# Kernel optimization log

Measured on AMD Instinct MI355X. Metric: run time of the kernel, lower is better.

Reference implementation:

```python
import jax, jax.numpy as jnp
import numpy as np

EPS = 1e-5   # BatchNorm3d eps
SLOPE = 0.01 # LeakyReLU default negative_slope

def conv3(x, w, pad):
    return jax.lax.conv_general_dilated(
        x, w, (1, 1, 1), [(pad, pad)] * 3,
        dimension_numbers=('NCDHW', 'OIDHW', 'NCDHW'))

def bn(x):
    # BatchNorm3d in training mode with affine init (weight=1, bias=0):
    # normalize by per-channel batch statistics (biased variance).
    m = x.mean(axis=(0, 2, 3, 4), keepdims=True)
    v = x.var(axis=(0, 2, 3, 4), keepdims=True)
    return (x - m) / jnp.sqrt(v + EPS)

def lrelu(x):
    return jnp.where(x >= 0, x, SLOPE * x)

def block(x, w1, w2):
    # ConvBlock: conv3x3x3 -> BN -> LeakyReLU, twice
    x = lrelu(bn(conv3(x, w1, 1)))
    return lrelu(bn(conv3(x, w2, 1)))

def maxpool2(x):
    # MaxPool3dMPS(kernel=2, stride=2, pad=0) == standard 2x2x2 maxpool
    B, C, D, H, W = x.shape
    return x.reshape(B, C, D // 2, 2, H // 2, 2, W // 2, 2).max(axis=(3, 5, 7))

def upconv_fft(x, w):
    # ConvTranspose3dMPS: nearest-neighbor upsample by stride=2 via repeat,
    # then per-(out,in)-channel CIRCULAR convolution implemented with FFTs
    # (weight zero-padded to the upsampled spatial shape). Vectorized here
    # over all channel pairs with a frequency-domain einsum; rfft is used
    # since all signals are real (identical math, half the memory).
    s = 2
    B, C, D, H, W = x.shape
    up = jnp.broadcast_to(x[:, :, :, None, :, None, :, None],
                          (B, C, D, s, H, s, W, s)).reshape(B, C, D * s, H * s, W * s)
    sp = up.shape[2:]
    X = jnp.fft.rfftn(up, axes=(2, 3, 4))                 # [B, Cin, D', H', Wf]
    Wf = jnp.fft.rfftn(w, s=sp, axes=(2, 3, 4))           # [Cout, Cin, D', H', Wf]
    Y = jnp.einsum('bidhw,oidhw->bodhw', X, Wf)
    return jnp.fft.irfftn(Y, s=sp, axes=(2, 3, 4))

def unet_fwd(x, wf1, wf2, wd1a, wd1b, wd2a, wd2b, wd3a, wd3b,
             wt1, wu1a, wu1b, wt2, wu2a, wu2b, wt3, wu3a, wu3b,
             w_final, b_final):
    x1 = block(x, wf1, wf2)                       # [B,16,64,64,64]
    x2 = block(maxpool2(x1), wd1a, wd1b)          # [B,32,32,32,32]
    x3 = block(maxpool2(x2), wd2a, wd2b)          # [B,64,16,16,16]
    x4 = block(maxpool2(x3), wd3a, wd3b)          # [B,128,8,8,8]

    def up(a, skip, wt, wa, wb):
        u = lrelu(bn(upconv_fft(a, wt)))
        return block(jnp.concatenate([skip, u], axis=1), wa, wb)

    a = up(x4, x3, wt1, wu1a, wu1b)               # [B,64,16,16,16]
    a = up(a, x2, wt2, wu2a, wu2b)                # [B,32,32,32,32]
    a = up(a, x1, wt3, wu3a, wu3b)                # [B,16,64,64,64]
    return conv3(a, w_final, 0) + b_final.reshape(1, -1, 1, 1, 1)

def setup_inputs() -> dict:
    key = jax.random.key(0)
    ks = jax.random.split(key, 32)
    def W(k, shape):
        fan = int(np.prod(shape[1:]))
        return jax.random.normal(k, shape, jnp.float32) * np.float32((2.0 / fan) ** 0.5)
    inp = {}
    inp['x'] = jax.random.normal(ks[0], (1, 1, 64, 64, 64), jnp.float32)
    shapes = {
        'wf1': (16, 1, 3, 3, 3),  'wf2': (16, 16, 3, 3, 3),
        'wd1a': (32, 16, 3, 3, 3), 'wd1b': (32, 32, 3, 3, 3),
        'wd2a': (64, 32, 3, 3, 3), 'wd2b': (64, 64, 3, 3, 3),
        'wd3a': (128, 64, 3, 3, 3), 'wd3b': (128, 128, 3, 3, 3),
        'wt1': (64, 128, 2, 2, 2), 'wu1a': (64, 128, 3, 3, 3), 'wu1b': (64, 64, 3, 3, 3),
        'wt2': (32, 64, 2, 2, 2),  'wu2a': (32, 64, 3, 3, 3),  'wu2b': (32, 32, 3, 3, 3),
        'wt3': (16, 32, 2, 2, 2),  'wu3a': (16, 32, 3, 3, 3),  'wu3b': (16, 16, 3, 3, 3),
        'w_final': (1, 16, 1, 1, 1),
    }
    for i, (name, sh) in enumerate(shapes.items()):
        inp[name] = W(ks[i + 1], sh)
    inp['b_final'] = jnp.zeros((1,), jnp.float32)
    return inp

def reference(x, wf1, wf2, wd1a, wd1b, wd2a, wd2b, wd3a, wd3b,
              wt1, wu1a, wu1b, wt2, wu2a, wu2b, wt3, wu3a, wu3b,
              w_final, b_final):
    return unet_fwd(x, wf1, wf2, wd1a, wd1b, wd2a, wd2b, wd3a, wd3b,
                    wt1, wu1a, wu1b, wt2, wu2a, wu2b, wt3, wu3a, wu3b,
                    w_final, b_final)
```

## Files before the change

### kernel.cpp

```cpp
#include <hip/hip_runtime.h>

#define EPS   1e-5f
#define SLOPE 0.01f

template <int CIN, int BT>
__global__ __launch_bounds__(BT) void conv3_big(const float* __restrict__ in,
                                                const float* __restrict__ wt,
                                                float* __restrict__ out,
                                                float* __restrict__ bstat,
                                                int D, int H, int W) {
    const int V   = D * H * W;
    const int NB  = gridDim.y;
    const int co0 = blockIdx.x * 8;
    __shared__ float wlds[27 * CIN * 8];
    __shared__ float sred[(BT / 64) * 16];
    for (int i = threadIdx.x; i < 27 * CIN * 8; i += BT) {
        const int co  = i & 7;
        const int r   = i >> 3;
        const int tap = r % 3;
        const int r2  = r / 3;
        const int pl  = r2 % 9;
        const int ci  = r2 / 9;
        wlds[i] = wt[((size_t)(co0 + co) * CIN + ci) * 27 + pl * 3 + tap];
    }
    __syncthreads();

    const int v0 = (blockIdx.y * BT + threadIdx.x) * 4;
    const int w0 = v0 % W;
    const int h0 = (v0 / W) % H;
    const int d0 = v0 / (W * H);
    const bool mL = (w0 != 0);
    const bool mR = (w0 + 4 != W);
    const int  wl = w0 - (mL ? 1 : 0);
    const int  wr = w0 + (mR ? 4 : 3);

    float acc[32];
#pragma unroll
    for (int i = 0; i < 32; ++i) acc[i] = 0.f;

#pragma unroll 1
    for (int ci = 0; ci < CIN; ++ci) {
        const float* pc = in + (size_t)ci * V;
#pragma unroll
        for (int kd = 0; kd < 3; ++kd) {
#pragma unroll
            for (int kh = 0; kh < 3; ++kh) {
                const int zd = d0 + kd - 1, zh = h0 + kh - 1;
                const bool okp = ((unsigned)zd < (unsigned)D) & ((unsigned)zh < (unsigned)H);
                const int row = okp ? (zd * H + zh) * W : 0;
                const float* p = pc + row;
                float4 m = *(const float4*)(p + w0);
                float lv = p[wl];
                float rv = p[wr];
                if (!okp) { m.x = 0.f; m.y = 0.f; m.z = 0.f; m.w = 0.f; }
                if (!(okp && mL)) lv = 0.f;
                if (!(okp && mR)) rv = 0.f;
                const float* wb = &wlds[((ci * 9 + kd * 3 + kh) * 3) * 8];
                const float4 t0a = *(const float4*)(wb);
                const float4 t0b = *(const float4*)(wb + 4);
                const float4 t1a = *(const float4*)(wb + 8);
                const float4 t1b = *(const float4*)(wb + 12);
                const float4 t2a = *(const float4*)(wb + 16);
                const float4 t2b = *(const float4*)(wb + 20);
#define FMA4C(A0, A1, A2, AP)                                                       \
                {                                                                   \
                    float* a = (AP);                                                \
                    a[0] = fmaf(lv,  (A0), fmaf(m.x, (A1), fmaf(m.y, (A2), a[0]))); \
                    a[1] = fmaf(m.x, (A0), fmaf(m.y, (A1), fmaf(m.z, (A2), a[1]))); \
                    a[2] = fmaf(m.y, (A0), fmaf(m.z, (A1), fmaf(m.w, (A2), a[2]))); \
                    a[3] = fmaf(m.z, (A0), fmaf(m.w, (A1), fmaf(rv,  (A2), a[3]))); \
                }
                FMA4C(t0a.x, t1a.x, t2a.x, acc + 0);
                FMA4C(t0a.y, t1a.y, t2a.y, acc + 4);
                FMA4C(t0a.z, t1a.z, t2a.z, acc + 8);
                FMA4C(t0a.w, t1a.w, t2a.w, acc + 12);
                FMA4C(t0b.x, t1b.x, t2b.x, acc + 16);
                FMA4C(t0b.y, t1b.y, t2b.y, acc + 20);
                FMA4C(t0b.z, t1b.z, t2b.z, acc + 24);
                FMA4C(t0b.w, t1b.w, t2b.w, acc + 28);
#undef FMA4C
            }
        }
    }
#pragma unroll
    for (int co = 0; co < 8; ++co)
        *(float4*)&out[(size_t)(co0 + co) * V + v0] = *(const float4*)&acc[co * 4];

    float s1[8], s2[8];
#pragma unroll
    for (int co = 0; co < 8; ++co) {
        const float* a = &acc[co * 4];
        s1[co] = a[0] + a[1] + a[2] + a[3];
        s2[co] = fmaf(a[0], a[0], fmaf(a[1], a[1], fmaf(a[2], a[2], a[3] * a[3])));
    }
#pragma unroll
    for (int off = 32; off > 0; off >>= 1)
#pragma unroll
        for (int co = 0; co < 8; ++co) {
            s1[co] += __shfl_down(s1[co], off, 64);
            s2[co] += __shfl_down(s2[co], off, 64);
        }
    const int lane = threadIdx.x & 63;
    const int wv   = threadIdx.x >> 6;
    if (lane == 0)
#pragma unroll
        for (int co = 0; co < 8; ++co) {
            sred[(wv * 8 + co) * 2]     = s1[co];
            sred[(wv * 8 + co) * 2 + 1] = s2[co];
        }
    __syncthreads();
    if ((int)threadIdx.x < 8) {
        float S1 = 0.f, S2 = 0.f;
#pragma unroll
        for (int w = 0; w < BT / 64; ++w) {
            S1 += sred[(w * 8 + threadIdx.x) * 2];
            S2 += sred[(w * 8 + threadIdx.x) * 2 + 1];
        }
        bstat[((size_t)(co0 + threadIdx.x) * NB + blockIdx.y) * 2]     = S1;
        bstat[((size_t)(co0 + threadIdx.x) * NB + blockIdx.y) * 2 + 1] = S2;
    }
}

template <int CIN>
__global__ __launch_bounds__(256) void upconv_big(const float* __restrict__ in,
                                                  const float* __restrict__ wt,
                                                  float* __restrict__ out,
                                                  float* __restrict__ bstat,
                                                  int Di, int Hi, int Wi) {
    const int Do = 2 * Di, Ho = 2 * Hi, Wo = 2 * Wi;
    const int Vo = Do * Ho * Wo;
    const int Vi = Di * Hi * Wi;
    const int NB = gridDim.y;
    const int co0 = blockIdx.x * 8;
    __shared__ float wlds[8 * CIN * 8];
    __shared__ float sred[4 * 16];
    for (int i = threadIdx.x; i < 8 * CIN * 8; i += 256) {
        const int co  = i & 7;
        const int t2  = i >> 3;
        const int ci  = t2 % CIN;
        const int tap = t2 / CIN;
        wlds[i] = wt[((size_t)(co0 + co) * CIN + ci) * 8 + tap];
    }
    __syncthreads();

    const int vbase = blockIdx.y * 1024 + threadIdx.x;
    int od[4], oh[4], ow[4];
#pragma unroll
    for (int j = 0; j < 4; ++j) {
        const int v = vbase + j * 256;
        ow[j] = v % Wo;
        oh[j] = (v / Wo) % Ho;
        od[j] = v / (Wo * Ho);
    }
    float acc[32];
#pragma unroll
    for (int i = 0; i < 32; ++i) acc[i] = 0.f;

#pragma unroll 1
    for (int kd = 0; kd < 2; ++kd)
#pragma unroll 1
    for (int kh = 0; kh < 2; ++kh)
#pragma unroll
    for (int kw = 0; kw < 2; ++kw) {
        const int tap = (kd * 2 + kh) * 2 + kw;
        int sp[4];
#pragma unroll
        for (int j = 0; j < 4; ++j) {
            const int id = ((od[j] - kd + Do) & (Do - 1)) >> 1;
            const int ih = ((oh[j] - kh + Ho) & (Ho - 1)) >> 1;
            const int iw = ((ow[j] - kw + Wo) & (Wo - 1)) >> 1;
            sp[j] = (id * Hi + ih) * Wi + iw;
        }
        const float* wrow = &wlds[tap * CIN * 8];
#pragma unroll 2
        for (int ci = 0; ci < CIN; ++ci) {
            float xv[4];
#pragma unroll
            for (int j = 0; j < 4; ++j)
                xv[j] = in[(size_t)ci * Vi + sp[j]];
            const float4 wa = *(const float4*)(wrow + ci * 8);
            const float4 wb = *(const float4*)(wrow + ci * 8 + 4);
#define UF(WC, CO)                                                              \
            {                                                                   \
                _Pragma("unroll")                                               \
                for (int j = 0; j < 4; ++j)                                     \
                    acc[(CO) * 4 + j] = fmaf(xv[j], (WC), acc[(CO) * 4 + j]);   \
            }
            UF(wa.x, 0) UF(wa.y, 1) UF(wa.z, 2) UF(wa.w, 3)
            UF(wb.x, 4) UF(wb.y, 5) UF(wb.z, 6) UF(wb.w, 7)
#undef UF
        }
    }
#pragma unroll
    for (int co = 0; co < 8; ++co)
#pragma unroll
        for (int j = 0; j < 4; ++j)
            out[(size_t)(co0 + co) * Vo + vbase + j * 256] = acc[co * 4 + j];

    float s1[8], s2[8];
#pragma unroll
    for (int co = 0; co < 8; ++co) {
        const float* a = &acc[co * 4];
        s1[co] = a[0] + a[1] + a[2] + a[3];
        s2[co] = fmaf(a[0], a[0], fmaf(a[1], a[1], fmaf(a[2], a[2], a[3] * a[3])));
    }
#pragma unroll
    for (int off = 32; off > 0; off >>= 1)
#pragma unroll
        for (int co = 0; co < 8; ++co) {
            s1[co] += __shfl_down(s1[co], off, 64);
            s2[co] += __shfl_down(s2[co], off, 64);
        }
    const int lane = threadIdx.x & 63;
    const int wv   = threadIdx.x >> 6;
    if (lane == 0)
#pragma unroll
        for (int co = 0; co < 8; ++co) {
            sred[(wv * 8 + co) * 2]     = s1[co];
            sred[(wv * 8 + co) * 2 + 1] = s2[co];
        }
    __syncthreads();
    if ((int)threadIdx.x < 8) {
        float S1 = 0.f, S2 = 0.f;
#pragma unroll
        for (int w = 0; w < 4; ++w) {
            S1 += sred[(w * 8 + threadIdx.x) * 2];
            S2 += sred[(w * 8 + threadIdx.x) * 2 + 1];
        }
        bstat[((size_t)(co0 + threadIdx.x) * NB + blockIdx.y) * 2]     = S1;
        bstat[((size_t)(co0 + threadIdx.x) * NB + blockIdx.y) * 2 + 1] = S2;
    }
}

__global__ __launch_bounds__(256) void bn_apply_f(const float* __restrict__ prt,
                                                  float* __restrict__ dst,
                                                  const float* __restrict__ bstat,
                                                  int NB, int V4, float invV) {
    const int c = blockIdx.x;
    float s1 = 0.f, s2 = 0.f;
    for (int i = threadIdx.x; i < NB; i += 256) {
        s1 += bstat[((size_t)c * NB + i) * 2];
        s2 += bstat[((size_t)c * NB + i) * 2 + 1];
    }
#pragma unroll
    for (int off = 32; off > 0; off >>= 1) {
        s1 += __shfl_down(s1, off, 64);
        s2 += __shfl_down(s2, off, 64);
    }
    __shared__ float sh[8];
    __shared__ float mv[2];
    const int lane = threadIdx.x & 63;
    const int wv   = threadIdx.x >> 6;
    if (lane == 0) { sh[wv] = s1; sh[4 + wv] = s2; }
    __syncthreads();
    if (threadIdx.x == 0) {
        const float S1 = sh[0] + sh[1] + sh[2] + sh[3];
        const float S2 = sh[4] + sh[5] + sh[6] + sh[7];
        const float mean = S1 * invV;
        const float var  = S2 * invV - mean * mean;
        mv[0] = mean;
        mv[1] = rsqrtf(var + EPS);
    }
    __syncthreads();
    const float mean = mv[0];
    const float rstd = mv[1];
    const int pos = blockIdx.y * 256 + threadIdx.x;
    float4 t = ((const float4*)prt)[(size_t)c * V4 + pos];
    float u;
    u = (t.x - mean) * rstd; t.x = u >= 0.f ? u : SLOPE * u;
    u = (t.y - mean) * rstd; t.y = u >= 0.f ? u : SLOPE * u;
    u = (t.z - mean) * rstd; t.z = u >= 0.f ? u : SLOPE * u;
    u = (t.w - mean) * rstd; t.w = u >= 0.f ? u : SLOPE * u;
    ((float4*)dst)[(size_t)c * V4 + pos] = t;
}

template <int CIN, int CC, int BT>
__global__ __launch_bounds__(BT) void conv3_qA(const float* __restrict__ in,
                                               const float* __restrict__ wt,
                                               float* __restrict__ part,
                                               int D, int H, int W) {
    const int V    = D * H * W;
    const int Cout = gridDim.x * 8;
    const int z    = blockIdx.z;
    const int cib  = z * CC;
    __shared__ float wlds[27 * CC * 8];
    const int co0 = blockIdx.x * 8;
    for (int i = threadIdx.x; i < 27 * CC * 8; i += BT) {
        const int co  = i & 7;
        const int t2  = i >> 3;
        const int tap = t2 % 3;
        const int t3  = t2 / 3;
        const int ci  = t3 % CC;
        const int pl  = t3 / CC;
        wlds[i] = wt[((size_t)(co0 + co) * CIN + cib + ci) * 27 + pl * 3 + tap];
    }
    __syncthreads();

    const float* inz = in + (size_t)cib * V;
    const int v0 = (blockIdx.y * BT + threadIdx.x) * 4;
    const int w0 = v0 % W;
    const int h0 = (v0 / W) % H;
    const int d0 = v0 / (W * H);

    const bool mL = (w0 != 0);
    const bool mR = (w0 + 4 != W);
    const int  wl = w0 - (mL ? 1 : 0);
    const int  wr = w0 + (mR ? 4 : 3);

    float acc[32];
#pragma unroll
    for (int i = 0; i < 32; ++i) acc[i] = 0.f;

#pragma unroll 1
    for (int kd = 0; kd < 3; ++kd) {
#pragma unroll 1
        for (int kh = 0; kh < 3; ++kh) {
            const int zd = d0 + kd - 1, zh = h0 + kh - 1;
            const bool okp = ((unsigned)zd < (unsigned)D) & ((unsigned)zh < (unsigned)H);
            const int row = okp ? (zd * H + zh) * W : 0;
            const float* wpl = &wlds[(kd * 3 + kh) * CC * 24];
#pragma unroll 2
            for (int ci = 0; ci < CC; ++ci) {
                const float* p = inz + (size_t)ci * V + row;
                float4 m = *(const float4*)(p + w0);
                float lv = p[wl];
                float rv = p[wr];
                if (!okp) { m.x = 0.f; m.y = 0.f; m.z = 0.f; m.w = 0.f; }
                if (!(okp && mL)) lv = 0.f;
                if (!(okp && mR)) rv = 0.f;
                const float* wb = wpl + ci * 24;
                const float4 t0a = *(const float4*)(wb);
                const float4 t0b = *(const float4*)(wb + 4);
                const float4 t1a = *(const float4*)(wb + 8);
                const float4 t1b = *(const float4*)(wb + 12);
                const float4 t2a = *(const float4*)(wb + 16);
                const float4 t2b = *(const float4*)(wb + 20);
#define FMA4C(A0, A1, A2, AP)                                                       \
                {                                                                   \
                    float* a = (AP);                                                \
                    a[0] = fmaf(lv,  (A0), fmaf(m.x, (A1), fmaf(m.y, (A2), a[0]))); \
                    a[1] = fmaf(m.x, (A0), fmaf(m.y, (A1), fmaf(m.z, (A2), a[1]))); \
                    a[2] = fmaf(m.y, (A0), fmaf(m.z, (A1), fmaf(m.w, (A2), a[2]))); \
                    a[3] = fmaf(m.z, (A0), fmaf(m.w, (A1), fmaf(rv,  (A2), a[3]))); \
                }
                FMA4C(t0a.x, t1a.x, t2a.x, acc + 0);
                FMA4C(t0a.y, t1a.y, t2a.y, acc + 4);
                FMA4C(t0a.z, t1a.z, t2a.z, acc + 8);
                FMA4C(t0a.w, t1a.w, t2a.w, acc + 12);
                FMA4C(t0b.x, t1b.x, t2b.x, acc + 16);
                FMA4C(t0b.y, t1b.y, t2b.y, acc + 20);
                FMA4C(t0b.z, t1b.z, t2b.z, acc + 24);
                FMA4C(t0b.w, t1b.w, t2b.w, acc + 28);
#undef FMA4C
            }
        }
    }
#pragma unroll
    for (int co = 0; co < 8; ++co)
        *(float4*)&part[((size_t)z * Cout + co0 + co) * V + v0] = *(const float4*)&acc[co * 4];
}

template <int CIN, int CC, int VOXB>
__global__ __launch_bounds__(256) void upconv_v8(const float* __restrict__ in,
                                                 const float* __restrict__ wt,
                                                 float* __restrict__ part,
                                                 int Di, int Hi, int Wi) {
    const int Do = 2 * Di, Ho = 2 * Hi, Wo = 2 * Wi;
    const int Vo = Do * Ho * Wo;
    const int Vi = Di * Hi * Wi;
    const int Cout = gridDim.x * 8;
    const int z    = blockIdx.z;
    const int cib  = z * CC;
    __shared__ float wlds[8 * CC * 8];
    const int co0 = blockIdx.x * 8;
    for (int i = threadIdx.x; i < 8 * CC * 8; i += 256) {
        const int co  = i & 7;
        const int t2  = i >> 3;
        const int ci  = t2 % CC;
        const int tap = t2 / CC;
        wlds[i] = wt[((size_t)(co0 + co) * CIN + cib + ci) * 8 + tap];
    }
    __syncthreads();

    const float* inz = in + (size_t)cib * Vi;
    const int vbase = blockIdx.y * (256 * VOXB) + threadIdx.x;
    int od[VOXB], oh[VOXB], ow[VOXB];
#pragma unroll
    for (int j = 0; j < VOXB; ++j) {
        const int v = vbase + j * 256;
        ow[j] = v % Wo;
        oh[j] = (v / Wo) % Ho;
        od[j] = v / (Wo * Ho);
    }
    float acc[8 * VOXB];
#pragma unroll
    for (int i = 0; i < 8 * VOXB; ++i) acc[i] = 0.f;

#pragma unroll 1
    for (int kd = 0; kd < 2; ++kd)
#pragma unroll 1
    for (int kh = 0; kh < 2; ++kh)
#pragma unroll
    for (int kw = 0; kw < 2; ++kw) {
        const int tap = (kd * 2 + kh) * 2 + kw;
        int sp[VOXB];
#pragma unroll
        for (int j = 0; j < VOXB; ++j) {
            const int id = ((od[j] - kd + Do) & (Do - 1)) >> 1;
            const int ih = ((oh[j] - kh + Ho) & (Ho - 1)) >> 1;
            const int iw = ((ow[j] - kw + Wo) & (Wo - 1)) >> 1;
            sp[j] = (id * Hi + ih) * Wi + iw;
        }
        const float* wrow = &wlds[tap * CC * 8];
#pragma unroll 2
        for (int ci = 0; ci < CC; ++ci) {
            float xv[VOXB];
#pragma unroll
            for (int j = 0; j < VOXB; ++j)
                xv[j] = inz[(size_t)ci * Vi + sp[j]];
            const float4 wa = *(const float4*)(wrow + ci * 8);
            const float4 wb = *(const float4*)(wrow + ci * 8 + 4);
#define UF(WC, CO)                                                              \
            {                                                                   \
                _Pragma("unroll")                                               \
                for (int j = 0; j < VOXB; ++j)                                  \
                    acc[(CO) * VOXB + j] = fmaf(xv[j], (WC), acc[(CO) * VOXB + j]); \
            }
            UF(wa.x, 0) UF(wa.y, 1) UF(wa.z, 2) UF(wa.w, 3)
            UF(wb.x, 4) UF(wb.y, 5) UF(wb.z, 6) UF(wb.w, 7)
#undef UF
        }
    }
#pragma unroll
    for (int co = 0; co < 8; ++co)
#pragma unroll
        for (int j = 0; j < VOXB; ++j)
            part[((size_t)z * Cout + co0 + co) * Vo + vbase + j * 256] = acc[co * VOXB + j];
}

__global__ __launch_bounds__(256) void bn_stats_part_v2(const float* __restrict__ part,
                                                        float* __restrict__ pstat,
                                                        int C, int V, int S, int chunk) {
    const int c = blockIdx.x, seg = blockIdx.y;
    const size_t base = (size_t)c * V + (size_t)seg * chunk;
    float s1 = 0.f, s2 = 0.f;
    for (int i = threadIdx.x * 4; i < chunk; i += 1024) {
        float4 t = make_float4(0.f, 0.f, 0.f, 0.f);
        for (int s = 0; s < S; ++s) {
            const float4 v = *(const float4*)(part + (size_t)s * C * V + base + i);
            t.x += v.x; t.y += v.y; t.z += v.z; t.w += v.w;
        }
        s1 += t.x + t.y + t.z + t.w;
        s2 = fmaf(t.x, t.x, fmaf(t.y, t.y, fmaf(t.z, t.z, fmaf(t.w, t.w, s2))));
    }
#pragma unroll
    for (int off = 32; off > 0; off >>= 1) {
        s1 += __shfl_down(s1, off, 64);
        s2 += __shfl_down(s2, off, 64);
    }
    __shared__ float sh[8];
    const int wid  = threadIdx.x >> 6;
    const int lane = threadIdx.x & 63;
    if (lane == 0) { sh[wid] = s1; sh[4 + wid] = s2; }
    __syncthreads();
    if (threadIdx.x == 0) {
        pstat[(c * gridDim.y + seg) * 2]     = sh[0] + sh[1] + sh[2] + sh[3];
        pstat[(c * gridDim.y + seg) * 2 + 1] = sh[4] + sh[5] + sh[6] + sh[7];
    }
}

__global__ __launch_bounds__(64) void bn_stats_final(const float* __restrict__ pstat,
                                                     float* __restrict__ stats,
                                                     int S, int V) {
    const int c = blockIdx.x;
    float s1 = 0.f, s2 = 0.f;
    if ((int)threadIdx.x < S) {
        s1 = pstat[(c * S + threadIdx.x) * 2];
        s2 = pstat[(c * S + threadIdx.x) * 2 + 1];
    }
#pragma unroll
    for (int off = 32; off > 0; off >>= 1) {
        s1 += __shfl_down(s1, off, 64);
        s2 += __shfl_down(s2, off, 64);
    }
    if (threadIdx.x == 0) {
        const float inv  = 1.f / (float)V;
        const float mean = s1 * inv;
        const float var  = s2 * inv - mean * mean;
        stats[2 * c]     = mean;
        stats[2 * c + 1] = rsqrtf(var + EPS);
    }
}

__global__ __launch_bounds__(256) void bn_apply_v3(const float* __restrict__ part,
                                                   float* __restrict__ dst,
                                                   const float* __restrict__ stats,
                                                   int C, int V4, int S, int total4) {
    const int idx = blockIdx.x * blockDim.x + threadIdx.x;
    if (idx >= total4) return;
    const int c = idx / V4;
    const int v = idx - c * V4;
    const float4* p4 = (const float4*)part;
    float4 t = make_float4(0.f, 0.f, 0.f, 0.f);
    for (int s = 0; s < S; ++s) {
        const float4 x = p4[(size_t)(s * C + c) * V4 + v];
        t.x += x.x; t.y += x.y; t.z += x.z; t.w += x.w;
    }
    const float mean = stats[2 * c];
    const float rstd = stats[2 * c + 1];
    float u;
    u = (t.x - mean) * rstd; t.x = u >= 0.f ? u : SLOPE * u;
    u = (t.y - mean) * rstd; t.y = u >= 0.f ? u : SLOPE * u;
    u = (t.z - mean) * rstd; t.z = u >= 0.f ? u : SLOPE * u;
    u = (t.w - mean) * rstd; t.w = u >= 0.f ? u : SLOPE * u;
    ((float4*)dst)[idx] = t;
}

__global__ __launch_bounds__(256) void maxpool_kernel(const float* __restrict__ in,
                                                      float* __restrict__ out,
                                                      int D, int H, int W, int total) {
    const int Do = D >> 1, Ho = H >> 1, Wo = W >> 1;
    const int Vo = Do * Ho * Wo;
    const int idx = blockIdx.x * blockDim.x + threadIdx.x;
    if (idx >= total) return;
    const int c  = idx / Vo;
    const int v  = idx - c * Vo;
    const int ow = v % Wo;
    const int oh = (v / Wo) % Ho;
    const int od = v / (Wo * Ho);
    const size_t HW = (size_t)H * W;
    const float* p = in + (size_t)c * D * HW + (size_t)(2 * od) * HW + (size_t)(2 * oh) * W + 2 * ow;
    float m = p[0];
    m = fmaxf(m, p[1]);
    m = fmaxf(m, p[W]);
    m = fmaxf(m, p[W + 1]);
    m = fmaxf(m, p[HW]);
    m = fmaxf(m, p[HW + 1]);
    m = fmaxf(m, p[HW + W]);
    m = fmaxf(m, p[HW + W + 1]);
    out[idx] = m;
}

__global__ __launch_bounds__(256) void final_v2(const float* __restrict__ in,
                                                const float* __restrict__ w,
                                                const float* __restrict__ b,
                                                float* __restrict__ out, int C, int V4) {
    const int idx = blockIdx.x * blockDim.x + threadIdx.x;
    if (idx >= V4) return;
    const float bb = b[0];
    float4 acc = make_float4(bb, bb, bb, bb);
    for (int c = 0; c < C; ++c) {
        const float4 v = ((const float4*)in)[(size_t)c * V4 + idx];
        const float wc = w[c];
        acc.x = fmaf(v.x, wc, acc.x);
        acc.y = fmaf(v.y, wc, acc.y);
        acc.z = fmaf(v.z, wc, acc.z);
        acc.w = fmaf(v.w, wc, acc.w);
    }
    ((float4*)out)[idx] = acc;
}


extern "C" void kernel_launch(void* const* d_in, const int* in_sizes, int n_in,
                              void* d_out, int out_size, void* d_ws, size_t ws_size,
                              hipStream_t stream) {
    const float* x      = (const float*)d_in[0];
    const float* wf1    = (const float*)d_in[1];
    const float* wf2    = (const float*)d_in[2];
    const float* wd1a   = (const float*)d_in[3];
    const float* wd1b   = (const float*)d_in[4];
    const float* wd2a   = (const float*)d_in[5];
    const float* wd2b   = (const float*)d_in[6];
    const float* wd3a   = (const float*)d_in[7];
    const float* wd3b   = (const float*)d_in[8];
    const float* wt1    = (const float*)d_in[9];
    const float* wu1a   = (const float*)d_in[10];
    const float* wu1b   = (const float*)d_in[11];
    const float* wt2    = (const float*)d_in[12];
    const float* wu2a   = (const float*)d_in[13];
    const float* wu2b   = (const float*)d_in[14];
    const float* wt3    = (const float*)d_in[15];
    const float* wu3a   = (const float*)d_in[16];
    const float* wu3b   = (const float*)d_in[17];
    const float* w_fin  = (const float*)d_in[18];
    const float* b_fin  = (const float*)d_in[19];
    float* out = (float*)d_out;

    const int V0 = 64 * 64 * 64;
    const int V1 = 32 * 32 * 32;
    const int V2 = 16 * 16 * 16;
    const int V3 = 8 * 8 * 8;

    float* ws    = (float*)d_ws;
    float* cat3  = ws;
    float* cat2  = cat3 + (size_t)32 * V0;
    float* cat1  = cat2 + (size_t)64 * V1;
    float* x4    = cat1 + (size_t)128 * V2;
    float* tA    = x4   + (size_t)128 * V3;
    float* tB    = tA   + (size_t)16 * V0;
    float* part  = tB   + (size_t)16 * V0;
    float* stats = part + (size_t)16 * V0;
    float* pstat = stats + 256;
    float* bstat = pstat + 4096;

    auto blocks = [](int n) { return (n + 255) / 256; };

    auto bn_lrelu = [&](const float* p, float* dstp, int C, int V, int S) {
        const int NSEG = (V >= V0) ? 16 : (V == V1) ? 8 : (V == V2) ? 2 : 1;
        hipLaunchKernelGGL(bn_stats_part_v2, dim3(C, NSEG), dim3(256), 0, stream,
                           p, pstat, C, V, S, V / NSEG);
        hipLaunchKernelGGL(bn_stats_final, dim3(C), dim3(64), 0, stream, pstat, stats, NSEG, V);
        const int total4 = C * V / 4;
        hipLaunchKernelGGL(bn_apply_v3, dim3(blocks(total4)), dim3(256), 0, stream,
                           p, dstp, stats, C, V / 4, S, total4);
    };
    auto maxpool = [&](const float* in, float* o, int C, int D, int H, int W) {
        const int total = C * (D / 2) * (H / 2) * (W / 2);
        hipLaunchKernelGGL(maxpool_kernel, dim3(blocks(total)), dim3(256), 0, stream,
                           in, o, D, H, W, total);
    };

#define CONVBIG(CIN, in_, wt_, prt_, dst_, Cout)                                            \
    {                                                                                       \
        const int NBv = V0 / (4 * 128);                                                     \
        dim3 g((Cout) / 8, NBv);                                                            \
        hipLaunchKernelGGL((conv3_big<CIN, 128>), g, dim3(128), 0, stream,                  \
                           in_, wt_, prt_, bstat, 64, 64, 64);                              \
        hipLaunchKernelGGL(bn_apply_f, dim3(Cout, V0 / 4 / 256), dim3(256), 0, stream,      \
                           prt_, dst_, bstat, NBv, V0 / 4, 1.f / V0);                       \
    }
#define CONVQ(CIN, CC, BT, in_, wt_, prt_, dst_, Cout, D_, H_, W_)                          \
    {                                                                                       \
        const int V_ = (D_) * (H_) * (W_);                                                  \
        const int S  = (CIN) / (CC);                                                        \
        dim3 g((Cout) / 8, V_ / (4 * (BT)), S);                                             \
        hipLaunchKernelGGL((conv3_qA<CIN, CC, BT>), g, dim3(BT), 0, stream,                 \
                           in_, wt_, prt_, D_, H_, W_);                                     \
        bn_lrelu(prt_, dst_, Cout, V_, S);                                                  \
    }
#define UPCONV(CIN, CC, VOXB, in_, wt_, prt_, dst_, Cout, Di_, Hi_, Wi_)                    \
    {                                                                                       \
        const int Vo_ = 8 * (Di_) * (Hi_) * (Wi_);                                          \
        const int S  = (CIN) / (CC);                                                        \
        dim3 g((Cout) / 8, Vo_ / (256 * (VOXB)), S);                                        \
        hipLaunchKernelGGL((upconv_v8<CIN, CC, VOXB>), g, dim3(256), 0, stream,             \
                           in_, wt_, prt_, Di_, Hi_, Wi_);                                  \
        bn_lrelu(prt_, dst_, Cout, Vo_, S);                                                 \
    }

    CONVBIG(1,  x,  wf1, tA, tA,   16);
    CONVBIG(16, tA, wf2, tB, cat3, 16);
    maxpool(cat3, tA, 16, 64, 64, 64);
    CONVQ(16,  8,  64,  tA,  wd1a, part, tB,          32, 32, 32, 32);
    CONVQ(32,  8,  64,  tB,  wd1b, part, cat2,        32, 32, 32, 32);
    maxpool(cat2, tA, 32, 32, 32, 32);
    CONVQ(32,  8,  64,  tA,  wd2a, part, tB,          64, 16, 16, 16);
    CONVQ(64,  8,  64,  tB,  wd2b, part, cat1,        64, 16, 16, 16);
    maxpool(cat1, tA, 64, 16, 16, 16);
    CONVQ(64,  4,  64,  tA,  wd3a, part, tB,         128, 8, 8, 8);
    CONVQ(128, 8,  64,  tB,  wd3b, part, x4,         128, 8, 8, 8);

    UPCONV(128, 16, 1, x4, wt1, part, cat1 + (size_t)64 * V2, 64, 8, 8, 8);
    CONVQ(128, 8,  64, cat1, wu1a, part, tA,          64, 16, 16, 16);
    CONVQ(64,  8,  64, tA,   wu1b, part, tB,          64, 16, 16, 16);

    UPCONV(64, 16, 1, tB, wt2, part, cat2 + (size_t)32 * V1, 32, 16, 16, 16);
    CONVQ(64, 16, 64, cat2, wu2a, part, tA,           32, 32, 32, 32);
    CONVQ(32, 8,  64, tA,   wu2b, part, tB,           32, 32, 32, 32);

    {
        float* up3dst = cat3 + (size_t)16 * V0;
        const int NBv = V0 / 1024;
        dim3 g(2, NBv);
        hipLaunchKernelGGL((upconv_big<32>), g, dim3(256), 0, stream,
                           tB, wt3, up3dst, bstat, 32, 32, 32);
        hipLaunchKernelGGL(bn_apply_f, dim3(16, V0 / 4 / 256), dim3(256), 0, stream,
                           up3dst, up3dst, bstat, NBv, V0 / 4, 1.f / V0);
    }
    CONVBIG(32, cat3, wu3a, tB,   tA, 16);
    CONVBIG(16, tA,   wu3b, cat3, tB, 16);

    hipLaunchKernelGGL(final_v2, dim3(blocks(V0 / 4)), dim3(256), 0, stream,
                       tB, w_fin, b_fin, out, 16, V0 / 4);

#undef CONVBIG
#undef CONVQ
#undef UPCONV
}
```

Baseline: 1.098 ms.

## Stage conv input halo tiles in LDS and fold BN stat finalize into apply

The 64^3 3x3x3 conv kernel now cooperatively loads a 3x10x64 input halo tile per input channel into shared memory. All 9 row taps then read neighbours from LDS instead of issuing separate global loads, at the cost of two barriers per channel. Separately, the bn_stats_final launch is removed: each bn_apply thread re-reduces the per-segment partial sums and computes mean and rstd itself. This saves one launch per BN but adds redundant small loads in every thread.

```diff
diff --git a/kernel.cpp b/kernel.cpp
--- a/kernel.cpp
+++ b/kernel.cpp
@@ -3,18 +3,18 @@
 #define EPS   1e-5f
 #define SLOPE 0.01f
 
-template <int CIN, int BT>
-__global__ __launch_bounds__(BT) void conv3_big(const float* __restrict__ in,
-                                                const float* __restrict__ wt,
-                                                float* __restrict__ out,
-                                                float* __restrict__ bstat,
-                                                int D, int H, int W) {
-    const int V   = D * H * W;
+template <int CIN>
+__global__ __launch_bounds__(128) void conv3_big(const float* __restrict__ in,
+                                                 const float* __restrict__ wt,
+                                                 float* __restrict__ out,
+                                                 float* __restrict__ bstat) {
+    const int V   = 64 * 64 * 64;
     const int NB  = gridDim.y;
     const int co0 = blockIdx.x * 8;
     __shared__ float wlds[27 * CIN * 8];
-    __shared__ float sred[(BT / 64) * 16];
-    for (int i = threadIdx.x; i < 27 * CIN * 8; i += BT) {
+    __shared__ float tile[3][10][64];
+    __shared__ float sred[2 * 16];
+    for (int i = threadIdx.x; i < 27 * CIN * 8; i += 128) {
         const int co  = i & 7;
         const int r   = i >> 3;
         const int tap = r % 3;
@@ -23,16 +23,15 @@
         const int ci  = r2 / 9;
         wlds[i] = wt[((size_t)(co0 + co) * CIN + ci) * 27 + pl * 3 + tap];
     }
-    __syncthreads();
-
-    const int v0 = (blockIdx.y * BT + threadIdx.x) * 4;
-    const int w0 = v0 % W;
-    const int h0 = (v0 / W) % H;
-    const int d0 = v0 / (W * H);
+
+    const int vb    = blockIdx.y * 512;
+    const int d0    = vb >> 12;
+    const int hbase = (vb >> 6) & 63;
+    const int hh0   = threadIdx.x >> 4;
+    const int w0    = (threadIdx.x & 15) * 4;
+    const int v0    = vb + (hh0 * 64) + w0;
     const bool mL = (w0 != 0);
-    const bool mR = (w0 + 4 != W);
-    const int  wl = w0 - (mL ? 1 : 0);
-    const int  wr = w0 + (mR ? 4 : 3);
+    const bool mR = (w0 + 4 != 64);
 
     float acc[32];
 #pragma unroll
@@ -40,21 +39,33 @@
 
 #pragma unroll 1
     for (int ci = 0; ci < CIN; ++ci) {
+        __syncthreads();
         const float* pc = in + (size_t)ci * V;
 #pragma unroll
+        for (int t = 0; t < 4; ++t) {
+            const int idx = threadIdx.x + t * 128;
+            if (idx < 480) {
+                const int r  = idx >> 4;
+                const int wq = (idx & 15) * 4;
+                const int kd = r / 10;
+                const int hh = r - kd * 10;
+                const int zd = d0 + kd - 1;
+                const int zh = hbase + hh - 1;
+                float4 val = make_float4(0.f, 0.f, 0.f, 0.f);
+                if (((unsigned)zd < 64u) & ((unsigned)zh < 64u))
+                    val = *(const float4*)(pc + ((zd << 6) + zh) * 64 + wq);
+                *(float4*)&tile[kd][hh][wq] = val;
+            }
+        }
+        __syncthreads();
+#pragma unroll
         for (int kd = 0; kd < 3; ++kd) {
 #pragma unroll
             for (int kh = 0; kh < 3; ++kh) {
-                const int zd = d0 + kd - 1, zh = h0 + kh - 1;
-                const bool okp = ((unsigned)zd < (unsigned)D) & ((unsigned)zh < (unsigned)H);
-                const int row = okp ? (zd * H + zh) * W : 0;
-                const float* p = pc + row;
-                float4 m = *(const float4*)(p + w0);
-                float lv = p[wl];
-                float rv = p[wr];
-                if (!okp) { m.x = 0.f; m.y = 0.f; m.z = 0.f; m.w = 0.f; }
-                if (!(okp && mL)) lv = 0.f;
-                if (!(okp && mR)) rv = 0.f;
+                const float* trow = &tile[kd][hh0 + kh][0];
+                const float4 m = *(const float4*)(trow + w0);
+                const float lv = mL ? trow[w0 - 1] : 0.f;
+                const float rv = mR ? trow[w0 + 4] : 0.f;
                 const float* wb = &wlds[((ci * 9 + kd * 3 + kh) * 3) * 8];
                 const float4 t0a = *(const float4*)(wb);
                 const float4 t0b = *(const float4*)(wb + 4);
@@ -112,7 +123,7 @@
     if ((int)threadIdx.x < 8) {
         float S1 = 0.f, S2 = 0.f;
 #pragma unroll
-        for (int w = 0; w < BT / 64; ++w) {
+        for (int w = 0; w < 2; ++w) {
             S1 += sred[(w * 8 + threadIdx.x) * 2];
             S2 += sred[(w * 8 + threadIdx.x) * 2 + 1];
         }
@@ -469,45 +480,29 @@
     }
 }
 
-__global__ __launch_bounds__(64) void bn_stats_final(const float* __restrict__ pstat,
-                                                     float* __restrict__ stats,
-                                                     int S, int V) {
-    const int c = blockIdx.x;
-    float s1 = 0.f, s2 = 0.f;
-    if ((int)threadIdx.x < S) {
-        s1 = pstat[(c * S + threadIdx.x) * 2];
-        s2 = pstat[(c * S + threadIdx.x) * 2 + 1];
-    }
-#pragma unroll
-    for (int off = 32; off > 0; off >>= 1) {
-        s1 += __shfl_down(s1, off, 64);
-        s2 += __shfl_down(s2, off, 64);
-    }
-    if (threadIdx.x == 0) {
-        const float inv  = 1.f / (float)V;
-        const float mean = s1 * inv;
-        const float var  = s2 * inv - mean * mean;
-        stats[2 * c]     = mean;
-        stats[2 * c + 1] = rsqrtf(var + EPS);
-    }
-}
-
-__global__ __launch_bounds__(256) void bn_apply_v3(const float* __restrict__ part,
+__global__ __launch_bounds__(256) void bn_apply_v4(const float* __restrict__ part,
                                                    float* __restrict__ dst,
-                                                   const float* __restrict__ stats,
-                                                   int C, int V4, int S, int total4) {
+                                                   const float* __restrict__ pstat,
+                                                   int C, int V4, int S, int NSEG,
+                                                   float invV, int total4) {
     const int idx = blockIdx.x * blockDim.x + threadIdx.x;
     if (idx >= total4) return;
     const int c = idx / V4;
     const int v = idx - c * V4;
+    float s1 = 0.f, s2 = 0.f;
+    for (int g = 0; g < NSEG; ++g) {
+        s1 += pstat[(c * NSEG + g) * 2];
+        s2 += pstat[(c * NSEG + g) * 2 + 1];
+    }
+    const float mean = s1 * invV;
+    const float var  = s2 * invV - mean * mean;
+    const float rstd = rsqrtf(var + EPS);
     const float4* p4 = (const float4*)part;
     float4 t = make_float4(0.f, 0.f, 0.f, 0.f);
     for (int s = 0; s < S; ++s) {
         const float4 x = p4[(size_t)(s * C + c) * V4 + v];
         t.x += x.x; t.y += x.y; t.z += x.z; t.w += x.w;
     }
-    const float mean = stats[2 * c];
-    const float rstd = stats[2 * c + 1];
     float u;
     u = (t.x - mean) * rstd; t.x = u >= 0.f ? u : SLOPE * u;
     u = (t.y - mean) * rstd; t.y = u >= 0.f ? u : SLOPE * u;
@@ -599,8 +594,7 @@
     float* tA    = x4   + (size_t)128 * V3;
     float* tB    = tA   + (size_t)16 * V0;
     float* part  = tB   + (size_t)16 * V0;
-    float* stats = part + (size_t)16 * V0;
-    float* pstat = stats + 256;
+    float* pstat = part + (size_t)16 * V0;
     float* bstat = pstat + 4096;
 
     auto blocks = [](int n) { return (n + 255) / 256; };
@@ -609,10 +603,9 @@
         const int NSEG = (V >= V0) ? 16 : (V == V1) ? 8 : (V == V2) ? 2 : 1;
         hipLaunchKernelGGL(bn_stats_part_v2, dim3(C, NSEG), dim3(256), 0, stream,
                            p, pstat, C, V, S, V / NSEG);
-        hipLaunchKernelGGL(bn_stats_final, dim3(C), dim3(64), 0, stream, pstat, stats, NSEG, V);
         const int total4 = C * V / 4;
-        hipLaunchKernelGGL(bn_apply_v3, dim3(blocks(total4)), dim3(256), 0, stream,
-                           p, dstp, stats, C, V / 4, S, total4);
+        hipLaunchKernelGGL(bn_apply_v4, dim3(blocks(total4)), dim3(256), 0, stream,
+                           p, dstp, pstat, C, V / 4, S, NSEG, 1.f / V, total4);
     };
     auto maxpool = [&](const float* in, float* o, int C, int D, int H, int W) {
         const int total = C * (D / 2) * (H / 2) * (W / 2);
@@ -622,10 +615,10 @@
 
 #define CONVBIG(CIN, in_, wt_, prt_, dst_, Cout)                                            \
     {                                                                                       \
-        const int NBv = V0 / (4 * 128);                                                     \
+        const int NBv = V0 / 512;                                                           \
         dim3 g((Cout) / 8, NBv);                                                            \
-        hipLaunchKernelGGL((conv3_big<CIN, 128>), g, dim3(128), 0, stream,                  \
-                           in_, wt_, prt_, bstat, 64, 64, 64);                              \
+        hipLaunchKernelGGL((conv3_big<CIN>), g, dim3(128), 0, stream,                       \
+                           in_, wt_, prt_, bstat);                                          \
         hipLaunchKernelGGL(bn_apply_f, dim3(Cout, V0 / 4 / 256), dim3(256), 0, stream,      \
                            prt_, dst_, bstat, NBv, V0 / 4, 1.f / V0);                       \
     }
```

Result: slower. 1.129 ms (+2.7%).
